# Kernel tuning notes

Measured on AMD Instinct MI355X. Metric: run time of the kernel, lower is better.

The kernel has to match this reference:

```python
import jax, jax.numpy as jnp
import numpy as np

WS = 7  # window_size


def setup_inputs() -> dict:
    key = jax.random.key(0)
    ks = jax.random.split(key, 4)
    B, C, H, W = 4, 384, 56, 56
    NH = 12
    x = jax.random.normal(ks[0], (B, C, H, W), dtype=jnp.float32)
    # 1x1 conv weights act as per-pixel linear maps over channels
    w_qkv = jax.random.normal(ks[1], (3 * C, C), dtype=jnp.float32) * (C ** -0.5)
    b_qkv = jnp.zeros((3 * C,), dtype=jnp.float32)
    w_proj = jax.random.normal(ks[2], (C, C), dtype=jnp.float32) * (C ** -0.5)
    b_proj = jnp.zeros((C,), dtype=jnp.float32)
    rel_bias = jax.random.normal(ks[3], (NH, WS, WS), dtype=jnp.float32) * 0.02
    return {"x": x, "w_qkv": w_qkv, "b_qkv": b_qkv,
            "w_proj": w_proj, "b_proj": b_proj, "rel_bias": rel_bias}


def reference(x, w_qkv, b_qkv, w_proj, b_proj, rel_bias):
    # Neighborhood attention: each query (i,j) attends to a ws x ws window of
    # keys/values centered at (i,j); borders handled by replication padding
    # (ReplicationPad2d), with a learned relative position bias (nh, ws, ws).
    B, C, H, W = x.shape
    nh, ws, _ = rel_bias.shape
    hd = C // nh
    p = ws // 2
    scale = hd ** -0.5

    # qkv 1x1 conv -> (B, 3, nh, hd, H, W)
    qkv = jnp.einsum('oc,bchw->bohw', w_qkv, x) + b_qkv[None, :, None, None]
    qkv = qkv.reshape(B, 3, nh, hd, H, W)
    q, k, v = qkv[:, 0] * scale, qkv[:, 1], qkv[:, 2]

    pad = ((0, 0), (0, 0), (0, 0), (p, p), (p, p))
    k_pad = jnp.pad(k, pad, mode='edge')  # replication padding
    v_pad = jnp.pad(v, pad, mode='edge')

    # attention logits over the ws*ws window offsets: (B, nh, H, W, K)
    logits = jnp.stack(
        [jnp.einsum('bnchw,bnchw->bnhw', q, k_pad[..., di:di + H, dj:dj + W])
         for di in range(ws) for dj in range(ws)], axis=-1)
    logits = logits + rel_bias.reshape(nh, ws * ws)[None, :, None, None, :]
    attn = jax.nn.softmax(logits, axis=-1)  # (attn_drop is identity in eval)

    # value windows: (B, nh, K, hd, H, W)
    v_win = jnp.stack([v_pad[..., di:di + H, dj:dj + W]
                       for di in range(ws) for dj in range(ws)], axis=2)
    out = jnp.einsum('bnhwk,bnkchw->bnchw', attn, v_win).reshape(B, C, H, W)

    # output projection 1x1 conv (proj_drop is identity in eval)
    out = jnp.einsum('oc,bchw->bohw', w_proj, out) + b_proj[None, :, None, None]
    return out
```

## Files before the change

kernel.cpp:

```cpp
#include <hip/hip_runtime.h>
#include <hip/hip_bf16.h>
#include <hip/hip_fp16.h>

#define S_HW 3136
#define SP   3200
#define IMG_W 56
#define C_DIM 384
#define NH_DIM 12
#define QKV_C 1152

#define TB 16
#define HALO 22
#define NPX 484
#define PLANE_B 3880

typedef float f32x4 __attribute__((ext_vector_type(4)));
typedef short bf16x8 __attribute__((ext_vector_type(8)));
typedef _Float16 f16x2 __attribute__((ext_vector_type(2)));

__device__ __forceinline__ void gld_lds16(const void* g, void* lds) {
    __builtin_amdgcn_global_load_lds(
        (const __attribute__((address_space(1))) void*)g,
        (__attribute__((address_space(3))) void*)lds, 16, 0, 0);
}

__device__ __forceinline__ float u2f(unsigned int u) { return __uint_as_float(u); }
__device__ __forceinline__ unsigned int f2bf_bits(float f) {
    unsigned int u = __float_as_uint(f);
    u += 0x7FFF + ((u >> 16) & 1);
    return u >> 16;
}
__device__ __forceinline__ unsigned int f2h_bits(float f) {
    return (unsigned int)__half_as_ushort(__float2half(f));
}

__global__ __launch_bounds__(256) void convert_w2_kernel(
    const float* __restrict__ a, int na, __hip_bfloat16* __restrict__ oa,
    const float* __restrict__ b, int nb, __hip_bfloat16* __restrict__ ob)
{
    int i = blockIdx.x * 256 + threadIdx.x;
    if (i < na) oa[i] = __float2bfloat16(a[i]);
    else if (i < na + nb) ob[i - na] = __float2bfloat16(b[i - na]);
}

__global__ __launch_bounds__(256) void transpose_convert_kernel(
    const float* __restrict__ x, __hip_bfloat16* __restrict__ xt)
{
    __shared__ float t[32][33];
    const int b = blockIdx.z;
    const int c0 = blockIdx.y * 32, s0 = blockIdx.x * 32;
    const int tid = threadIdx.x;

    const int lc = tid >> 3, ls = (tid & 7) * 4;
    float4 v = *reinterpret_cast<const float4*>(
        &x[((size_t)b * C_DIM + c0 + lc) * S_HW + s0 + ls]);
    t[lc][ls + 0] = v.x; t[lc][ls + 1] = v.y;
    t[lc][ls + 2] = v.z; t[lc][ls + 3] = v.w;
    __syncthreads();

    const int ws = tid >> 3, wc = (tid & 7) * 4;
    uint2 pk;
    pk.x = f2bf_bits(t[wc + 0][ws]) | (f2bf_bits(t[wc + 1][ws]) << 16);
    pk.y = f2bf_bits(t[wc + 2][ws]) | (f2bf_bits(t[wc + 3][ws]) << 16);
    *reinterpret_cast<uint2*>(
        &xt[((size_t)b * SP + s0 + ws) * C_DIM + c0 + wc]) = pk;
}

template <bool TRANS_OUT, int NF, typename OutT>
__global__ __launch_bounds__(256) void gemm_bf16_mfma(
    const __hip_bfloat16* __restrict__ A,
    const __hip_bfloat16* __restrict__ Bt,
    const float* __restrict__ bias,
    OutT* __restrict__ Y,
    int O, int K, float qscale, int qrows)
{
    constexpr int BN = NF * 32;
    __shared__ char smem[16384 + BN * 128];
    char* As0 = smem;
    char* As1 = smem + 8192;
    char* Bs0 = smem + 16384;
    char* Bs1 = smem + 16384 + BN * 64;

    const int b   = blockIdx.z;
    const int m0  = blockIdx.y * 128;
    const int n0  = blockIdx.x * BN;
    const int tid = threadIdx.x;
    const int w = tid >> 6, l = tid & 63;
    const int wr = w >> 1, wc = w & 1;

    const int srow = l >> 2;
    const int skk  = (l & 3) * 8;

    const __hip_bfloat16* Bb = Bt + (size_t)b * SP * K;

    f32x4 acc[4][NF];
    #pragma unroll
    for (int i = 0; i < 4; ++i)
        #pragma unroll
        for (int j = 0; j < NF; ++j) {
            f32x4 z = {0.f, 0.f, 0.f, 0.f};
            acc[i][j] = z;
        }

    const int frow = l & 15;
    const int fk   = (l >> 4) * 16;

    for (int k0 = 0; k0 < K; k0 += 64) {
        #pragma unroll
        for (int j = 0; j < 2; ++j) {
            const int chunk = w * 2 + j;
            const int m = chunk * 16 + srow;
            gld_lds16(A + (size_t)(m0 + m) * K + k0 + skk,      As0 + chunk * 1024);
            gld_lds16(A + (size_t)(m0 + m) * K + k0 + 32 + skk, As1 + chunk * 1024);
        }
        if (NF == 4) {
            #pragma unroll
            for (int j = 0; j < 2; ++j) {
                const int chunk = w * 2 + j;
                const int m = chunk * 16 + srow;
                gld_lds16(Bb + (size_t)(n0 + m) * K + k0 + skk,      Bs0 + chunk * 1024);
                gld_lds16(Bb + (size_t)(n0 + m) * K + k0 + 32 + skk, Bs1 + chunk * 1024);
            }
        } else {
            const int m = w * 16 + srow;
            gld_lds16(Bb + (size_t)(n0 + m) * K + k0 + skk,      Bs0 + w * 1024);
            gld_lds16(Bb + (size_t)(n0 + m) * K + k0 + 32 + skk, Bs1 + w * 1024);
        }
        __syncthreads();
        {
            bf16x8 af[4], bfr[NF];
            #pragma unroll
            for (int mi = 0; mi < 4; ++mi)
                af[mi] = *reinterpret_cast<const bf16x8*>(
                    As0 + (wr * 64 + mi * 16 + frow) * 64 + fk);
            #pragma unroll
            for (int ni = 0; ni < NF; ++ni)
                bfr[ni] = *reinterpret_cast<const bf16x8*>(
                    Bs0 + (wc * (NF * 16) + ni * 16 + frow) * 64 + fk);
            #pragma unroll
            for (int mi = 0; mi < 4; ++mi)
                #pragma unroll
                for (int ni = 0; ni < NF; ++ni)
                    acc[mi][ni] = __builtin_amdgcn_mfma_f32_16x16x32_bf16(
                        af[mi], bfr[ni], acc[mi][ni], 0, 0, 0);
        }
        {
            bf16x8 af[4], bfr[NF];
            #pragma unroll
            for (int mi = 0; mi < 4; ++mi)
                af[mi] = *reinterpret_cast<const bf16x8*>(
                    As1 + (wr * 64 + mi * 16 + frow) * 64 + fk);
            #pragma unroll
            for (int ni = 0; ni < NF; ++ni)
                bfr[ni] = *reinterpret_cast<const bf16x8*>(
                    Bs1 + (wc * (NF * 16) + ni * 16 + frow) * 64 + fk);
            #pragma unroll
            for (int mi = 0; mi < 4; ++mi)
                #pragma unroll
                for (int ni = 0; ni < NF; ++ni)
                    acc[mi][ni] = __builtin_amdgcn_mfma_f32_16x16x32_bf16(
                        af[mi], bfr[ni], acc[mi][ni], 0, 0, 0);
        }
        __syncthreads();
    }

    const int crow0 = (l >> 4) * 4;
    const int ccol  = l & 15;
    if (TRANS_OUT) {
        __hip_bfloat16* Yb = (__hip_bfloat16*)Y + (size_t)b * SP * O;
        #pragma unroll
        for (int ni = 0; ni < NF; ++ni) {
            const int col = n0 + wc * (NF * 16) + ni * 16 + ccol;
            if (col >= S_HW) continue;
            #pragma unroll
            for (int mi = 0; mi < 4; ++mi) {
                const int row0 = m0 + wr * 64 + mi * 16 + crow0;
                const float sc = (row0 < qrows) ? qscale : 1.f;
                float v0 = (acc[mi][ni][0] + bias[row0 + 0]) * sc;
                float v1 = (acc[mi][ni][1] + bias[row0 + 1]) * sc;
                float v2 = (acc[mi][ni][2] + bias[row0 + 2]) * sc;
                float v3 = (acc[mi][ni][3] + bias[row0 + 3]) * sc;
                uint2 pk;
                pk.x = f2h_bits(v0) | (f2h_bits(v1) << 16);
                pk.y = f2h_bits(v2) | (f2h_bits(v3) << 16);
                *reinterpret_cast<uint2*>(&Yb[(size_t)col * O + row0]) = pk;
            }
        }
    } else {
        float* Yb = (float*)Y + (size_t)b * O * S_HW;
        #pragma unroll
        for (int ni = 0; ni < NF; ++ni) {
            const int col = n0 + wc * (NF * 16) + ni * 16 + ccol;
            if (col >= S_HW) continue;
            #pragma unroll
            for (int mi = 0; mi < 4; ++mi) {
                #pragma unroll
                for (int r = 0; r < 4; ++r) {
                    const int row = m0 + wr * 64 + mi * 16 + crow0 + r;
                    float v = acc[mi][ni][r] + bias[row];
                    if (row < qrows) v *= qscale;
                    Yb[(size_t)row * S_HW + col] = v;
                }
            }
        }
    }
}

__global__ __launch_bounds__(256, 2) void na_attn_kernel(
    const __hip_bfloat16* __restrict__ qkvt, const float* __restrict__ rel_bias,
    __hip_bfloat16* __restrict__ outt)
{
    __shared__ alignas(16) char halo[8 * PLANE_B];

    const int blk  = blockIdx.x;
    const int tile = blk & 15;
    const int bn   = blk >> 4;
    const int nh   = bn % NH_DIM;
    const int b    = bn / NH_DIM;
    const int th0  = (tile >> 2) * TB;
    const int tw0  = (tile & 3) * TB;

    const int tid = threadIdx.x;
    const int ty = tid >> 4, tx = tid & 15;
    const int h = th0 + ty, w = tw0 + tx;
    const bool valid = (h < 56) && (w < 56);
    const int s = h * IMG_W + w;

    const __hip_bfloat16* base = qkvt + (size_t)b * SP * QKV_C;
    const int co = nh * 32;

    #pragma unroll
    for (int i = 0; i < 8; ++i) {
        const int idx = tid + i * 256;
        if (idx < NPX * 4) {
            const int px = idx >> 2, g = idx & 3;
            const int hy = px / HALO, hx = px - hy * HALO;
            const int y = min(max(th0 - 3 + hy, 0), 55);
            const int x = min(max(tw0 - 3 + hx, 0), 55);
            const uint4 v = *reinterpret_cast<const uint4*>(
                base + (size_t)(y * IMG_W + x) * QKV_C + C_DIM + co + g * 8);
            uint2 lo; lo.x = v.x; lo.y = v.y;
            uint2 hi; hi.x = v.z; hi.y = v.w;
            *reinterpret_cast<uint2*>(&halo[(2 * g + 0) * PLANE_B + px * 8]) = lo;
            *reinterpret_cast<uint2*>(&halo[(2 * g + 1) * PLANE_B + px * 8]) = hi;
        }
    }

    unsigned int qreg[16];
    if (valid) {
        const uint4* qp = reinterpret_cast<const uint4*>(base + (size_t)s * QKV_C + co);
        #pragma unroll
        for (int g = 0; g < 4; ++g) {
            uint4 qg = qp[g];
            qreg[4 * g + 0] = qg.x; qreg[4 * g + 1] = qg.y;
            qreg[4 * g + 2] = qg.z; qreg[4 * g + 3] = qg.w;
        }
    }
    __syncthreads();

    float logits[49];
    if (valid) {
        #pragma unroll
        for (int di = 0; di < 7; ++di) {
            #pragma unroll
            for (int dj = 0; dj < 7; ++dj) {
                const int hp = (ty + di) * HALO + (tx + dj);
                const char* hb = halo + hp * 8;
                float acc0 = 0.f, acc1 = 0.f;
                #pragma unroll
                for (int pl = 0; pl < 8; ++pl) {
                    uint2 kk = *reinterpret_cast<const uint2*>(hb + pl * PLANE_B);
#if __has_builtin(__builtin_amdgcn_fdot2)
                    acc0 = __builtin_amdgcn_fdot2(
                        __builtin_bit_cast(f16x2, qreg[2 * pl]),
                        __builtin_bit_cast(f16x2, kk.x), acc0, false);
                    acc1 = __builtin_amdgcn_fdot2(
                        __builtin_bit_cast(f16x2, qreg[2 * pl + 1]),
                        __builtin_bit_cast(f16x2, kk.y), acc1, false);
#else
                    f16x2 qa = __builtin_bit_cast(f16x2, qreg[2 * pl]);
                    f16x2 qb = __builtin_bit_cast(f16x2, qreg[2 * pl + 1]);
                    f16x2 ka = __builtin_bit_cast(f16x2, kk.x);
                    f16x2 kb = __builtin_bit_cast(f16x2, kk.y);
                    acc0 += (float)qa[0] * (float)ka[0] + (float)qa[1] * (float)ka[1];
                    acc1 += (float)qb[0] * (float)kb[0] + (float)qb[1] * (float)kb[1];
#endif
                }
                logits[di * 7 + dj] = acc0 + acc1 + rel_bias[(nh * 7 + di) * 7 + dj];
            }
        }
    }
    __syncthreads();

    #pragma unroll
    for (int i = 0; i < 8; ++i) {
        const int idx = tid + i * 256;
        if (idx < NPX * 4) {
            const int px = idx >> 2, g = idx & 3;
            const int hy = px / HALO, hx = px - hy * HALO;
            const int y = min(max(th0 - 3 + hy, 0), 55);
            const int x = min(max(tw0 - 3 + hx, 0), 55);
            const uint4 v = *reinterpret_cast<const uint4*>(
                base + (size_t)(y * IMG_W + x) * QKV_C + 2 * C_DIM + co + g * 8);
            uint2 lo; lo.x = v.x; lo.y = v.y;
            uint2 hi; hi.x = v.z; hi.y = v.w;
            *reinterpret_cast<uint2*>(&halo[(2 * g + 0) * PLANE_B + px * 8]) = lo;
            *reinterpret_cast<uint2*>(&halo[(2 * g + 1) * PLANE_B + px * 8]) = hi;
        }
    }

    unsigned int ppk[25];
    float inv = 0.f;
    if (valid) {
        float mx = logits[0];
        #pragma unroll
        for (int i = 1; i < 49; ++i) mx = fmaxf(mx, logits[i]);
        float sum = 0.f;
        #pragma unroll
        for (int i = 0; i < 24; ++i) {
            float e0 = __expf(logits[2 * i] - mx);
            float e1 = __expf(logits[2 * i + 1] - mx);
            sum += e0 + e1;
            ppk[i] = f2bf_bits(e0) << 16 | f2bf_bits(e1);
        }
        {
            float e0 = __expf(logits[48] - mx);
            sum += e0;
            ppk[24] = f2bf_bits(e0) << 16;
        }
        inv = 1.f / sum;
    }
    __syncthreads();

    if (valid) {
        float o[32];
        #pragma unroll
        for (int c = 0; c < 32; ++c) o[c] = 0.f;

        #pragma unroll
        for (int n = 0; n < 49; ++n) {
            const unsigned int pu = ppk[n >> 1];
            const float pv = (n & 1) ? u2f(pu << 16) : u2f(pu & 0xFFFF0000u);
            const int di = n / 7, dj = n % 7;
            const int hp = (ty + di) * HALO + (tx + dj);
            const char* hb = halo + hp * 8;
            #pragma unroll
            for (int pl = 0; pl < 8; ++pl) {
                uint2 vv = *reinterpret_cast<const uint2*>(hb + pl * PLANE_B);
                f16x2 va = __builtin_bit_cast(f16x2, vv.x);
                f16x2 vb = __builtin_bit_cast(f16x2, vv.y);
                o[4 * pl + 0] = fmaf((float)va[0], pv, o[4 * pl + 0]);
                o[4 * pl + 1] = fmaf((float)va[1], pv, o[4 * pl + 1]);
                o[4 * pl + 2] = fmaf((float)vb[0], pv, o[4 * pl + 2]);
                o[4 * pl + 3] = fmaf((float)vb[1], pv, o[4 * pl + 3]);
            }
        }

        uint4* dst = reinterpret_cast<uint4*>(outt + ((size_t)b * SP + s) * C_DIM + co);
        #pragma unroll
        for (int g = 0; g < 4; ++g) {
            uint4 pk;
            pk.x = f2bf_bits(o[8 * g + 0] * inv) | (f2bf_bits(o[8 * g + 1] * inv) << 16);
            pk.y = f2bf_bits(o[8 * g + 2] * inv) | (f2bf_bits(o[8 * g + 3] * inv) << 16);
            pk.z = f2bf_bits(o[8 * g + 4] * inv) | (f2bf_bits(o[8 * g + 5] * inv) << 16);
            pk.w = f2bf_bits(o[8 * g + 6] * inv) | (f2bf_bits(o[8 * g + 7] * inv) << 16);
            dst[g] = pk;
        }
    }
}

extern "C" void kernel_launch(void* const* d_in, const int* in_sizes, int n_in,
                              void* d_out, int out_size, void* d_ws, size_t ws_size,
                              hipStream_t stream) {
    const float* x        = (const float*)d_in[0];
    const float* w_qkv    = (const float*)d_in[1];
    const float* b_qkv    = (const float*)d_in[2];
    const float* w_proj   = (const float*)d_in[3];
    const float* b_proj   = (const float*)d_in[4];
    const float* rel_bias = (const float*)d_in[5];
    float* out = (float*)d_out;

    __hip_bfloat16* xt   = (__hip_bfloat16*)d_ws;
    __hip_bfloat16* wq   = xt + (size_t)4 * SP * C_DIM;
    __hip_bfloat16* wp   = wq + (size_t)QKV_C * C_DIM;
    __hip_bfloat16* qkvt = wp + (size_t)C_DIM * C_DIM;
    __hip_bfloat16* att  = qkvt + (size_t)4 * SP * QKV_C;

    const float scale = 0.17677669529663687f;
    const int nwq = QKV_C * C_DIM, nwp = C_DIM * C_DIM;

    convert_w2_kernel<<<dim3((nwq + nwp + 255) / 256), 256, 0, stream>>>(
        w_qkv, nwq, wq, w_proj, nwp, wp);
    transpose_convert_kernel<<<dim3(98, 12, 4), dim3(256), 0, stream>>>(x, xt);

    gemm_bf16_mfma<true, 4, __hip_bfloat16><<<dim3(25, 9, 4), 256, 0, stream>>>(
        wq, xt, b_qkv, qkvt, QKV_C, C_DIM, scale, C_DIM);

    na_attn_kernel<<<dim3(4 * NH_DIM * 16), 256, 0, stream>>>(qkvt, rel_bias, att);

    gemm_bf16_mfma<false, 2, float><<<dim3(50, 3, 4), 256, 0, stream>>>(
        wp, att, b_proj, out, C_DIM, C_DIM, 1.f, 0);
}
```

Before: 93.93 us.

## Merge weight conversion into transpose kernel and prefetch V halo during logits

Folds the weight bf16 conversion into the input transpose kernel as an extra grid slice, removing one kernel launch. In the attention kernel, half of the V halo tile is loaded into registers before the QK logits computation, so those global loads overlap with compute. The staged values are written to LDS after the barrier. This adds 16 live registers across the logits phase, which may lower occupancy.

```diff
diff --git a/kernel.cpp b/kernel.cpp
--- a/kernel.cpp
+++ b/kernel.cpp
@@ -34,22 +34,26 @@
     return (unsigned int)__half_as_ushort(__float2half(f));
 }
 
-__global__ __launch_bounds__(256) void convert_w2_kernel(
-    const float* __restrict__ a, int na, __hip_bfloat16* __restrict__ oa,
-    const float* __restrict__ b, int nb, __hip_bfloat16* __restrict__ ob)
+__global__ __launch_bounds__(256) void prep_kernel(
+    const float* __restrict__ x, __hip_bfloat16* __restrict__ xt,
+    const float* __restrict__ wa, int na, __hip_bfloat16* __restrict__ oa,
+    const float* __restrict__ wb, int nb, __hip_bfloat16* __restrict__ ob)
 {
-    int i = blockIdx.x * 256 + threadIdx.x;
-    if (i < na) oa[i] = __float2bfloat16(a[i]);
-    else if (i < na + nb) ob[i - na] = __float2bfloat16(b[i - na]);
-}
-
-__global__ __launch_bounds__(256) void transpose_convert_kernel(
-    const float* __restrict__ x, __hip_bfloat16* __restrict__ xt)
-{
+    const int tid = threadIdx.x;
+    if (blockIdx.z == 4) {
+        const int bid  = blockIdx.y * 98 + blockIdx.x;
+        const int base = bid * 512 + tid;
+        #pragma unroll
+        for (int r = 0; r < 2; ++r) {
+            const int i = base + r * 256;
+            if (i < na) oa[i] = __float2bfloat16(wa[i]);
+            else if (i < na + nb) ob[i - na] = __float2bfloat16(wb[i - na]);
+        }
+        return;
+    }
     __shared__ float t[32][33];
     const int b = blockIdx.z;
     const int c0 = blockIdx.y * 32, s0 = blockIdx.x * 32;
-    const int tid = threadIdx.x;
 
     const int lc = tid >> 3, ls = (tid & 7) * 4;
     float4 v = *reinterpret_cast<const float4*>(
@@ -244,6 +248,18 @@
             *reinterpret_cast<uint2*>(&halo[(2 * g + 0) * PLANE_B + px * 8]) = lo;
             *reinterpret_cast<uint2*>(&halo[(2 * g + 1) * PLANE_B + px * 8]) = hi;
         }
+    }
+
+    uint4 vstage[4];
+    #pragma unroll
+    for (int i = 0; i < 4; ++i) {
+        const int idx = tid + i * 256;
+        const int px = idx >> 2, g = idx & 3;
+        const int hy = px / HALO, hx = px - hy * HALO;
+        const int y = min(max(th0 - 3 + hy, 0), 55);
+        const int x = min(max(tw0 - 3 + hx, 0), 55);
+        vstage[i] = *reinterpret_cast<const uint4*>(
+            base + (size_t)(y * IMG_W + x) * QKV_C + 2 * C_DIM + co + g * 8);
     }
 
     unsigned int qreg[16];
@@ -293,7 +309,16 @@
     __syncthreads();
 
     #pragma unroll
-    for (int i = 0; i < 8; ++i) {
+    for (int i = 0; i < 4; ++i) {
+        const int idx = tid + i * 256;
+        const int px = idx >> 2, g = idx & 3;
+        uint2 lo; lo.x = vstage[i].x; lo.y = vstage[i].y;
+        uint2 hi; hi.x = vstage[i].z; hi.y = vstage[i].w;
+        *reinterpret_cast<uint2*>(&halo[(2 * g + 0) * PLANE_B + px * 8]) = lo;
+        *reinterpret_cast<uint2*>(&halo[(2 * g + 1) * PLANE_B + px * 8]) = hi;
+    }
+    #pragma unroll
+    for (int i = 4; i < 8; ++i) {
         const int idx = tid + i * 256;
         if (idx < NPX * 4) {
             const int px = idx >> 2, g = idx & 3;
@@ -389,9 +414,8 @@
     const float scale = 0.17677669529663687f;
     const int nwq = QKV_C * C_DIM, nwp = C_DIM * C_DIM;
 
-    convert_w2_kernel<<<dim3((nwq + nwp + 255) / 256), 256, 0, stream>>>(
-        w_qkv, nwq, wq, w_proj, nwp, wp);
-    transpose_convert_kernel<<<dim3(98, 12, 4), dim3(256), 0, stream>>>(x, xt);
+    prep_kernel<<<dim3(98, 12, 5), 256, 0, stream>>>(
+        x, xt, w_qkv, nwq, wq, w_proj, nwp, wp);
 
     gemm_bf16_mfma<true, 4, __hip_bfloat16><<<dim3(25, 9, 4), 256, 0, stream>>>(
         wq, xt, b_qkv, qkvt, QKV_C, C_DIM, scale, C_DIM);
```

Measured after the change: 89.38 us (median of 3 runs). 4.8% less time.
